# Kernel tuning notes

Hardware: AMD Instinct MI355X
Metric: run time of the kernel (lower is better)

Reference implementation:

```python
import jax, jax.numpy as jnp
import numpy as np

EPS = 1e-5  # nn.BatchNorm2d default eps


def _cbs(x, w, g, b, m, v):
    # Conv(k=1, bias=False) + BatchNorm2d(inference) + SiLU
    y = jnp.einsum('bchw,oc->bohw', x, w)
    s = (g * jax.lax.rsqrt(v + EPS))[None, :, None, None]
    y = (y - m[None, :, None, None]) * s + b[None, :, None, None]
    return y * jax.nn.sigmoid(y)


def setup_inputs():
    key = jax.random.key(0)
    B, D, H, W = 1, 256, 80, 80
    C = D // 2
    ks = jax.random.split(key, 20)
    r = lambda i, shape, sc=1.0: jax.random.normal(ks[i], shape, dtype=jnp.float32) * sc
    oC, oD = jnp.ones((C,), jnp.float32), jnp.ones((D,), jnp.float32)
    zC, zD = jnp.zeros((C,), jnp.float32), jnp.zeros((D,), jnp.float32)
    return {
        'x': r(0, (B, D, H, W)),
        'w1': r(1, (C, D), 0.05), 'g1': oC, 'b1': zC, 'm1': zC, 'v1': oC,
        'w2': r(2, (D, C), 0.05), 'g2': oD, 'b2': zD, 'm2': zD, 'v2': oD,
        'w3': r(3, (D, C), 0.05), 'g3': oD, 'b3': zD, 'm3': zD, 'v3': oD,
        'wq': r(4, (C, C), 0.05), 'bq': r(5, (C,), 0.01),
        'wk': r(6, (C, C), 0.05), 'bk': r(7, (C,), 0.01),
        'wv': r(8, (C, C), 0.05), 'bv': r(9, (C,), 0.01),
        'wp': r(10, (C, C), 0.05), 'bp': r(11, (C,), 0.01),
        'rel_h': r(12, (1, C, H, 1)), 'rel_w': r(13, (1, C, 1, W)),
        'ef_h': r(14, (1, C, H, 1)), 'ef_w': r(15, (1, C, 1, W)),
    }


def reference(x, w1, g1, b1, m1, v1, w2, g2, b2, m2, v2, w3, g3, b3, m3, v3,
              wq, bq, wk, bk, wv, bv, wp, bp, rel_h, rel_w, ef_h, ef_w):
    x1 = _cbs(x, w1, g1, b1, m1, v1)            # [B, C, H, W]
    B, C, H, W = x1.shape
    HW = H * W
    proj = lambda w, b: (jnp.einsum('bchw,oc->bohw', x1, w)
                         + b[None, :, None, None]).reshape(B, C, HW)
    q = proj(wq, bq)
    k = proj(wk, bk)
    v = proj(wv, bv)
    p = proj(wp, bp)
    # content-content + content-position attention branch
    cp = (rel_h + rel_w).reshape(C, HW)          # [C, HW]
    cc = jnp.einsum('bci,bcj->bij', q, k)        # [B, HW, HW]
    cpos = jnp.einsum('ci,bcj->bij', cp, q)      # [B, HW, HW]
    attn = jax.nn.softmax(cc + cpos, axis=-1)
    # out1[b,c,i] = sum_j v[b,c,j] * attn[b,i,j]  (bmm(v, attn^T))
    out1 = jnp.einsum('bcj,bij->bci', v, attn).reshape(B, C, H, W)
    # extra positional branch (valid because B == 1)
    ef = (ef_h + ef_w).reshape(B, C, HW)         # [1, C, HW]
    ce = jnp.einsum('bci,bcj->bij', p, ef)       # [B, HW, HW]
    eng = jax.nn.softmax(ce, axis=-1)
    out2 = jnp.einsum('bcj,bij->bci', ef, eng).reshape(B, C, H, W)
    return x + _cbs(out1, w2, g2, b2, m2, v2) + _cbs(out2, w3, g3, b3, m3, v3)
```

## Files before the change

kernel.cpp:

```cpp
#include <hip/hip_runtime.h>


typedef unsigned short u16;
typedef __attribute__((ext_vector_type(8))) short bf16x8;
typedef __attribute__((ext_vector_type(4))) float f32x4;
typedef __attribute__((ext_vector_type(4))) unsigned int u32x4;

#define HW 6400
#define BN_EPS 1e-5f

__device__ __forceinline__ u16 f2b(float f) {
  unsigned u = __float_as_uint(f);
  u += 0x7fffu + ((u >> 16) & 1u);
  return (u16)(u >> 16);
}
__device__ __forceinline__ unsigned pack2(float a, float b) {
  return (unsigned)f2b(a) | ((unsigned)f2b(b) << 16);
}
__device__ __forceinline__ f32x4 MFMA(bf16x8 a, bf16x8 b, f32x4 c) {
  return __builtin_amdgcn_mfma_f32_16x16x32_bf16(a, b, c, 0, 0, 0);
}
__device__ __forceinline__ float silu_f(float y) {
  return y / (1.0f + __expf(-y));
}
__device__ __forceinline__ bf16x8 pack8(f32x4 lo, f32x4 hi, float sc) {
  union { bf16x8 v; uint4 u; } r;
  r.u.x = pack2(lo[0] * sc, lo[1] * sc);
  r.u.y = pack2(lo[2] * sc, lo[3] * sc);
  r.u.z = pack2(hi[0] * sc, hi[1] * sc);
  r.u.w = pack2(hi[2] * sc, hi[3] * sc);
  return r.v;
}
__device__ __forceinline__ void gload_lds16(const u16* src, u16* dst) {
  __builtin_amdgcn_global_load_lds(
      (const __attribute__((address_space(1))) void*)src,
      (__attribute__((address_space(3))) void*)dst, 16, 0, 0);
}
__device__ __forceinline__ void lds_fence() {
  __builtin_amdgcn_sched_barrier(0);
  asm volatile("s_waitcnt lgkmcnt(0)" ::: "memory");
  __builtin_amdgcn_sched_barrier(0);
}

__global__ void prep_all(
    const float* __restrict__ rel_h, const float* __restrict__ rel_w,
    const float* __restrict__ ef_h, const float* __restrict__ ef_w,
    const float* __restrict__ w1, const float* __restrict__ g1, const float* __restrict__ b1,
    const float* __restrict__ m1, const float* __restrict__ v1,
    const float* __restrict__ w2, const float* __restrict__ g2, const float* __restrict__ b2,
    const float* __restrict__ m2, const float* __restrict__ v2,
    const float* __restrict__ w3, const float* __restrict__ g3, const float* __restrict__ b3,
    const float* __restrict__ m3, const float* __restrict__ v3,
    const float* __restrict__ wq, const float* __restrict__ bq,
    const float* __restrict__ wk, const float* __restrict__ bk,
    const float* __restrict__ wv, const float* __restrict__ bv,
    const float* __restrict__ wp, const float* __restrict__ bp,
    u16* __restrict__ LT,
    u16* __restrict__ w1b, float* __restrict__ b1e,
    u16* __restrict__ Wcat, float* __restrict__ bcat,
    u16* __restrict__ w2b, float* __restrict__ b2e,
    u16* __restrict__ w3b, float* __restrict__ b3e,
    u16* __restrict__ efhT, u16* __restrict__ efwT,
    u16* __restrict__ efhB, u16* __restrict__ efwB,
    u16* __restrict__ expA, u16* __restrict__ expB,
    float* __restrict__ lbuf)
{
  const int b = blockIdx.x;
  const int t = threadIdx.x;
  if (b < 80) {
    const int h = b;
    const int c0 = (t & 63) * 2;
    const float rh0 = rel_h[c0 * 80 + h], rh1 = rel_h[(c0 + 1) * 80 + h];
    for (int wcol = (t >> 6); wcol < 80; wcol += 4) {
      const int i = h * 80 + wcol;
      float rw0 = rel_w[c0 * 80 + wcol], rw1 = rel_w[(c0 + 1) * 80 + wcol];
      *(unsigned*)&LT[(size_t)i * 256 + 128 + c0] = pack2(rh0 + rw0, rh1 + rw1);
    }
  } else if (b < 144) {
    const int tid = (b - 80) * 256 + t;
    const int stride = 64 * 256;
    for (int idx = tid; idx < 128 * 256; idx += stride) {
      int o = idx >> 8;
      float s = g1[o] * rsqrtf(v1[o] + BN_EPS);
      w1b[idx] = f2b(w1[idx] * s);
    }
    for (int idx = tid; idx < 128; idx += stride) {
      float s = g1[idx] * rsqrtf(v1[idx] + BN_EPS);
      b1e[idx] = b1[idx] - m1[idx] * s;
    }
    for (int idx = tid; idx < 4 * 128 * 128; idx += stride) {
      int which = idx >> 14, r = idx & 16383;
      const float* src = which == 0 ? wq : which == 1 ? wk : which == 2 ? wv : wp;
      Wcat[idx] = f2b(src[r]);
    }
    for (int idx = tid; idx < 512; idx += stride) {
      int which = idx >> 7, r = idx & 127;
      const float* src = which == 0 ? bq : which == 1 ? bk : which == 2 ? bv : bp;
      bcat[idx] = src[r];
    }
    for (int idx = tid; idx < 256 * 128; idx += stride) {
      int o = idx >> 7;
      float s2 = g2[o] * rsqrtf(v2[o] + BN_EPS);
      w2b[idx] = f2b(w2[idx] * s2);
      float s3 = g3[o] * rsqrtf(v3[o] + BN_EPS);
      w3b[idx] = f2b(w3[idx] * s3);
    }
    for (int idx = tid; idx < 256; idx += stride) {
      float s2 = g2[idx] * rsqrtf(v2[idx] + BN_EPS);
      b2e[idx] = b2[idx] - m2[idx] * s2;
      float s3 = g3[idx] * rsqrtf(v3[idx] + BN_EPS);
      b3e[idx] = b3[idx] - m3[idx] * s3;
    }
    for (int idx = tid; idx < 80 * 128; idx += stride) {
      int hj = idx >> 7, c = idx & 127;
      efhT[idx] = f2b(ef_h[c * 80 + hj]);
      efwT[idx] = f2b(ef_w[c * 80 + hj]);
    }
    for (int idx = tid; idx < 128 * 96; idx += stride) {
      int c = idx / 96, hj = idx % 96;
      efhB[idx] = hj < 80 ? f2b(ef_h[c * 80 + hj]) : (u16)0;
      efwB[idx] = hj < 80 ? f2b(ef_w[c * 80 + hj]) : (u16)0;
    }
  } else {
    const int tid = (b - 144) * 256 + t;
    const int stride = 32 * 256;
    for (int idx = tid; idx < HW / 4; idx += stride)
      ((f32x4*)lbuf)[idx] = (f32x4){0.f, 0.f, 0.f, 0.f};
    for (int idx = tid; idx < HW * 96 / 8; idx += stride) {
      ((u32x4*)expA)[idx] = (u32x4){0, 0, 0, 0};
      ((u32x4*)expB)[idx] = (u32x4){0, 0, 0, 0};
    }
  }
}

__global__ __launch_bounds__(128) void front_k(
    const float* __restrict__ x,
    const u16* __restrict__ w1b, const float* __restrict__ b1e,
    const u16* __restrict__ Wcat, const float* __restrict__ bcat,
    u16* __restrict__ LT, u16* __restrict__ RT, u16* __restrict__ Vv,
    u16* __restrict__ pT)
{
  __shared__ __align__(16) u16 tr[2][16][136];
  const int t = threadIdx.x, w = t >> 6, lane = t & 63, jl = lane & 15, q = lane >> 4;
  const int i0 = blockIdx.x * 32 + w * 16;

  bf16x8 afr[8];
#pragma unroll
  for (int ks = 0; ks < 8; ++ks) {
    union { bf16x8 v; u16 e[8]; } fa;
#pragma unroll
    for (int e = 0; e < 8; ++e)
      fa.e[e] = f2b(x[(size_t)(ks * 32 + q * 8 + e) * HW + i0 + jl]);
    afr[ks] = fa.v;
  }
  f32x4 acc[8];
#pragma unroll
  for (int nf = 0; nf < 8; ++nf) acc[nf] = (f32x4){0.f, 0.f, 0.f, 0.f};
#pragma unroll
  for (int ks = 0; ks < 8; ++ks)
#pragma unroll
    for (int nf = 0; nf < 8; ++nf) {
      bf16x8 b = *(const bf16x8*)(w1b + (size_t)(nf * 16 + jl) * 256 + ks * 32 + q * 8);
      acc[nf] = MFMA(afr[ks], b, acc[nf]);
    }
#pragma unroll
  for (int nf = 0; nf < 8; ++nf) {
    const int c = nf * 16 + jl;
    const float bias = b1e[c];
#pragma unroll
    for (int r = 0; r < 4; ++r)
      tr[w][q * 4 + r][c] = f2b(silu_f(acc[nf][r] + bias));
  }
  __syncthreads();
  bf16x8 xa[4];
#pragma unroll
  for (int ks = 0; ks < 4; ++ks)
    xa[ks] = *(const bf16x8*)&tr[w][jl][ks * 32 + q * 8];

#pragma unroll
  for (int nc = 0; nc < 4; ++nc) {
    f32x4 a2[8];
#pragma unroll
    for (int nf = 0; nf < 8; ++nf) a2[nf] = (f32x4){0.f, 0.f, 0.f, 0.f};
#pragma unroll
    for (int ks = 0; ks < 4; ++ks)
#pragma unroll
      for (int nf = 0; nf < 8; ++nf) {
        bf16x8 b = *(const bf16x8*)(Wcat + (size_t)(nc * 128 + nf * 16 + jl) * 128 + ks * 32 + q * 8);
        a2[nf] = MFMA(xa[ks], b, a2[nf]);
      }
    if (nc == 2) {
#pragma unroll
      for (int nf = 0; nf < 8; ++nf) {
        const int c = nf * 16 + jl;
        const float bias = bcat[256 + c];
        uint2 pk;
        pk.x = pack2(a2[nf][0] + bias, a2[nf][1] + bias);
        pk.y = pack2(a2[nf][2] + bias, a2[nf][3] + bias);
        *(uint2*)(Vv + (size_t)c * HW + i0 + q * 4) = pk;
      }
    } else {
      __syncthreads();
#pragma unroll
      for (int nf = 0; nf < 8; ++nf) {
        const int c = nf * 16 + jl;
        const float bias = bcat[nc * 128 + c];
#pragma unroll
        for (int r = 0; r < 4; ++r)
          tr[w][q * 4 + r][c] = f2b(a2[nf][r] + bias);
      }
      __syncthreads();
#pragma unroll
      for (int r = 0; r < 16; ++r) {
        unsigned val = *(const unsigned*)&tr[w][r][lane * 2];
        const size_t row = (size_t)(i0 + r);
        if (nc == 0) {
          *(unsigned*)(LT + row * 256 + lane * 2) = val;
          *(unsigned*)(RT + row * 256 + 128 + lane * 2) = val;
        } else if (nc == 1) {
          *(unsigned*)(RT + row * 256 + lane * 2) = val;
        } else {
          *(unsigned*)(pT + row * 128 + lane * 2) = val;
        }
      }
    }
  }
}

__global__ __launch_bounds__(256) void sep2a(
    const u16* __restrict__ pT,
    const u16* __restrict__ efhT,
    const u16* __restrict__ efwT,
    u16* __restrict__ expA, u16* __restrict__ expB,
    float* __restrict__ sA, float* __restrict__ sB)
{
  const int t = threadIdx.x, lane = t & 63, w = t >> 6, jl = lane & 15, q = lane >> 4;
  const int i0w = blockIdx.x * 128 + w * 32;

  bf16x8 pfr[2][4];
#pragma unroll
  for (int mt = 0; mt < 2; ++mt)
#pragma unroll
    for (int l = 0; l < 4; ++l)
      pfr[mt][l] = *(const bf16x8*)(pT + (size_t)(i0w + mt * 16 + jl) * 128 + l * 32 + q * 8);

  f32x4 sa[5][2], sb[5][2];
#pragma unroll
  for (int nf = 0; nf < 5; ++nf)
#pragma unroll
    for (int mt = 0; mt < 2; ++mt) {
      sa[nf][mt] = (f32x4){0.f, 0.f, 0.f, 0.f};
      sb[nf][mt] = (f32x4){0.f, 0.f, 0.f, 0.f};
    }
#pragma unroll
  for (int nf = 0; nf < 5; ++nf) {
    const int row = nf * 16 + jl;
#pragma unroll
    for (int l = 0; l < 4; ++l) {
      bf16x8 eh = *(const bf16x8*)(efhT + (size_t)row * 128 + l * 32 + q * 8);
      bf16x8 ew = *(const bf16x8*)(efwT + (size_t)row * 128 + l * 32 + q * 8);
      sa[nf][0] = MFMA(eh, pfr[0][l], sa[nf][0]);
      sa[nf][1] = MFMA(eh, pfr[1][l], sa[nf][1]);
      sb[nf][0] = MFMA(ew, pfr[0][l], sb[nf][0]);
      sb[nf][1] = MFMA(ew, pfr[1][l], sb[nf][1]);
    }
  }
#pragma unroll
  for (int mt = 0; mt < 2; ++mt) {
    const int i = i0w + mt * 16 + jl;
    float ra = 0.f, rb = 0.f;
#pragma unroll
    for (int nf = 0; nf < 5; ++nf) {
      float ea[4], eb[4];
#pragma unroll
      for (int r = 0; r < 4; ++r) {
        ea[r] = __expf(sa[nf][mt][r]); ra += ea[r];
        eb[r] = __expf(sb[nf][mt][r]); rb += eb[r];
      }
      uint2 pa, pb;
      pa.x = pack2(ea[0], ea[1]); pa.y = pack2(ea[2], ea[3]);
      pb.x = pack2(eb[0], eb[1]); pb.y = pack2(eb[2], eb[3]);
      *(uint2*)(expA + (size_t)i * 96 + nf * 16 + q * 4) = pa;
      *(uint2*)(expB + (size_t)i * 96 + nf * 16 + q * 4) = pb;
    }
    ra += __shfl_xor(ra, 16); ra += __shfl_xor(ra, 32);
    rb += __shfl_xor(rb, 16); rb += __shfl_xor(rb, 32);
    if (lane < 16) { sA[i] = ra; sB[i] = rb; }
  }
}

__global__ __launch_bounds__(256) void sep2b(
    const u16* __restrict__ expA, const u16* __restrict__ expB,
    const float* __restrict__ sA, const float* __restrict__ sB,
    const u16* __restrict__ efhB, const u16* __restrict__ efwB,
    float* __restrict__ O2)
{
  const int t = threadIdx.x, lane = t & 63, w = t >> 6, jl = lane & 15, q = lane >> 4;
  const int i0w = blockIdx.x * 128 + w * 32;

#pragma unroll
  for (int mt = 0; mt < 2; ++mt) {
    bf16x8 fa[3], fb[3];
#pragma unroll
    for (int l = 0; l < 3; ++l) {
      fa[l] = *(const bf16x8*)(expA + (size_t)(i0w + mt * 16 + jl) * 96 + l * 32 + q * 8);
      fb[l] = *(const bf16x8*)(expB + (size_t)(i0w + mt * 16 + jl) * 96 + l * 32 + q * 8);
    }
    f32x4 oU[8], oW[8];
#pragma unroll
    for (int nf = 0; nf < 8; ++nf) {
      oU[nf] = (f32x4){0.f, 0.f, 0.f, 0.f};
      oW[nf] = (f32x4){0.f, 0.f, 0.f, 0.f};
    }
#pragma unroll
    for (int l = 0; l < 3; ++l)
#pragma unroll
      for (int nf = 0; nf < 8; ++nf) {
        bf16x8 bh = *(const bf16x8*)(efhB + (size_t)(nf * 16 + jl) * 96 + l * 32 + q * 8);
        bf16x8 bw = *(const bf16x8*)(efwB + (size_t)(nf * 16 + jl) * 96 + l * 32 + q * 8);
        oU[nf] = MFMA(fa[l], bh, oU[nf]);
        oW[nf] = MFMA(fb[l], bw, oW[nf]);
      }
    const int ib = i0w + mt * 16 + q * 4;
    float ia[4], iw[4];
#pragma unroll
    for (int r = 0; r < 4; ++r) {
      ia[r] = 1.0f / sA[ib + r];
      iw[r] = 1.0f / sB[ib + r];
    }
#pragma unroll
    for (int nf = 0; nf < 8; ++nf)
#pragma unroll
      for (int r = 0; r < 4; ++r)
        O2[(size_t)(ib + r) * 128 + nf * 16 + jl] = oU[nf][r] * ia[r] + oW[nf][r] * iw[r];
  }
}

__global__ __launch_bounds__(512) void fused_attn(
    const u16* __restrict__ LT,
    const u16* __restrict__ RT,
    const u16* __restrict__ Vv,
    float* __restrict__ Opart,
    float* __restrict__ lv)
{
  __shared__ __align__(1024) u16 Rs[2][128 * 128];
  __shared__ __align__(1024) u16 Ts[8][32 * 128];
  const int t = threadIdx.x, lane = t & 63, w = t >> 6, jl = lane & 15, q = lane >> 4;
  const int it = blockIdx.x / 10, jp = blockIdx.x % 10;
  const int i0w = it * 256 + w * 32;
  u16* T0 = Ts[w];
  u16* T1 = Ts[w] + 2048;

  bf16x8 afr[2][8];
#pragma unroll
  for (int mt = 0; mt < 2; ++mt)
#pragma unroll
    for (int l = 0; l < 8; ++l)
      afr[mt][l] = *(const bf16x8*)(LT + (size_t)(i0w + mt * 16 + jl) * 256 + l * 32 + q * 8);

  f32x4 o[2][8];
#pragma unroll
  for (int mt = 0; mt < 2; ++mt)
#pragma unroll
    for (int cf = 0; cf < 8; ++cf) o[mt][cf] = (f32x4){0.f, 0.f, 0.f, 0.f};
  float lacc[2] = {0.f, 0.f};

  auto stage = [&](int jj) {
#pragma unroll
    for (int k = 0; k < 8; ++k) {
      const int b = k >> 2, cl = k & 3;
      const int cc = w * 4 + cl;
      const int jr = cc * 4 + (lane >> 4);
      const int cp = lane & 15;
      const int ch = (cp & ~7) | ((cp ^ jr) & 7);
      gload_lds16(RT + (size_t)(jj + jr) * 256 + b * 128 + ch * 8,
                  Rs[b] + (cc << 9));
    }
  };

  stage(jp * 640);

  for (int stp = 0; stp < 5; ++stp) {
    const int jj = jp * 640 + stp * 128;

    f32x4 s[8][2];
#pragma unroll
    for (int nf = 0; nf < 8; ++nf)
#pragma unroll
      for (int mt = 0; mt < 2; ++mt) s[nf][mt] = (f32x4){0.f, 0.f, 0.f, 0.f};

    __syncthreads();

#pragma unroll
    for (int h = 0; h < 2; ++h)
#pragma unroll
      for (int nf = 0; nf < 8; ++nf) {
        const int row = nf * 16 + jl;
#pragma unroll
        for (int l = 0; l < 4; ++l) {
          const int ch = (l * 4 + q) ^ (jl & 7);
          bf16x8 b = *(const bf16x8*)(Rs[h] + row * 128 + ch * 8);
          s[nf][0] = MFMA(b, afr[0][h * 4 + l], s[nf][0]);
          s[nf][1] = MFMA(b, afr[1][h * 4 + l], s[nf][1]);
        }
      }
    __syncthreads();
    if (stp < 4) stage(jj + 128);

#pragma unroll
    for (int nf = 0; nf < 8; ++nf)
#pragma unroll
      for (int mt = 0; mt < 2; ++mt)
#pragma unroll
        for (int r = 0; r < 4; ++r) {
          float p = __expf(s[nf][mt][r]);
          s[nf][mt][r] = p;
          lacc[mt] += p;
        }

#pragma unroll
    for (int mt = 0; mt < 2; ++mt)
#pragma unroll
      for (int nf = 0; nf < 8; ++nf) {
        const int cs = (nf * 4 + q) ^ ((jl & 7) << 2);
        uint2 pk;
        pk.x = pack2(s[nf][mt][0], s[nf][mt][1]);
        pk.y = pack2(s[nf][mt][2], s[nf][mt][3]);
        *(uint2*)((mt ? T1 : T0) + jl * 128 + cs * 4) = pk;
      }
    lds_fence();

#pragma unroll
    for (int ks2 = 0; ks2 < 4; ++ks2) {
      const int cb = (ks2 * 8 + q * 2) ^ ((jl & 7) << 2);
      bf16x8 pa0 = *(const bf16x8*)(T0 + jl * 128 + cb * 4);
      bf16x8 pa1 = *(const bf16x8*)(T1 + jl * 128 + cb * 4);
#pragma unroll
      for (int cf = 0; cf < 8; ++cf) {
        bf16x8 bv = *(const bf16x8*)(Vv + (size_t)(cf * 16 + jl) * HW + jj + ks2 * 32 + q * 8);
        o[0][cf] = MFMA(pa0, bv, o[0][cf]);
        o[1][cf] = MFMA(pa1, bv, o[1][cf]);
      }
    }
  }

#pragma unroll
  for (int mt = 0; mt < 2; ++mt) {
    float rsum = lacc[mt];
    rsum += __shfl_xor(rsum, 16);
    rsum += __shfl_xor(rsum, 32);
    if (lane < 16)
      atomicAdd(&lv[i0w + mt * 16 + jl], rsum);
  }
  float* Op = Opart + (size_t)jp * HW * 128;
#pragma unroll
  for (int mt = 0; mt < 2; ++mt) {
    const int ib = i0w + mt * 16 + q * 4;
#pragma unroll
    for (int cf = 0; cf < 8; ++cf) {
      const int c = cf * 16 + jl;
#pragma unroll
      for (int r = 0; r < 4; ++r)
        Op[(size_t)(ib + r) * 128 + c] = o[mt][cf][r];
    }
  }
}

__global__ __launch_bounds__(256) void final_k(
    const float* __restrict__ Opart,
    const float* __restrict__ O2,
    const float* __restrict__ lbuf,
    const u16* __restrict__ w2b, const float* __restrict__ b2e,
    const u16* __restrict__ w3b, const float* __restrict__ b3e,
    const float* __restrict__ x, float* __restrict__ outp)
{
  const int t = threadIdx.x, w = t >> 6, lane = t & 63, jl = lane & 15, q = lane >> 4;
  const int i0 = blockIdx.x * 64 + w * 16;
  const int nc = blockIdx.y;
  const int row = i0 + jl;

  const float inv1 = 1.0f / lbuf[row];
  const float* O2r = O2 + (size_t)row * 128;

  f32x4 a1[8], a2[8];
#pragma unroll
  for (int nf = 0; nf < 8; ++nf) {
    a1[nf] = (f32x4){0.f, 0.f, 0.f, 0.f};
    a2[nf] = (f32x4){0.f, 0.f, 0.f, 0.f};
  }
#pragma unroll
  for (int ks = 0; ks < 4; ++ks) {
    f32x4 s1a = (f32x4){0.f, 0.f, 0.f, 0.f};
    f32x4 s1b = (f32x4){0.f, 0.f, 0.f, 0.f};
#pragma unroll
    for (int p = 0; p < 10; ++p) {
      const float* Or = Opart + ((size_t)p * HW + row) * 128;
      s1a += *(const f32x4*)(Or + ks * 32 + q * 8);
      s1b += *(const f32x4*)(Or + ks * 32 + q * 8 + 4);
    }
    f32x4 s2a = *(const f32x4*)(O2r + ks * 32 + q * 8);
    f32x4 s2b = *(const f32x4*)(O2r + ks * 32 + q * 8 + 4);
    bf16x8 fa1 = pack8(s1a, s1b, inv1);
    bf16x8 fa2 = pack8(s2a, s2b, 1.0f);
#pragma unroll
    for (int nf = 0; nf < 8; ++nf) {
      bf16x8 b2f = *(const bf16x8*)(w2b + (size_t)(nc * 128 + nf * 16 + jl) * 128 + ks * 32 + q * 8);
      bf16x8 b3f = *(const bf16x8*)(w3b + (size_t)(nc * 128 + nf * 16 + jl) * 128 + ks * 32 + q * 8);
      a1[nf] = MFMA(fa1, b2f, a1[nf]);
      a2[nf] = MFMA(fa2, b3f, a2[nf]);
    }
  }
#pragma unroll
  for (int nf = 0; nf < 8; ++nf) {
    const int d = nc * 128 + nf * 16 + jl;
    const float bb2 = b2e[d], bb3 = b3e[d];
    const size_t base = (size_t)d * HW + i0 + q * 4;
    f32x4 xv = *(const f32x4*)(x + base);
    f32x4 rv;
#pragma unroll
    for (int r = 0; r < 4; ++r)
      rv[r] = xv[r] + silu_f(a1[nf][r] + bb2) + silu_f(a2[nf][r] + bb3);
    *(f32x4*)(outp + base) = rv;
  }
}

extern "C" void kernel_launch(void* const* d_in, const int* in_sizes, int n_in,
                              void* d_out, int out_size, void* d_ws, size_t ws_size,
                              hipStream_t stream)
{
  (void)in_sizes; (void)n_in; (void)out_size; (void)ws_size;
  const float* x   = (const float*)d_in[0];
  const float* w1  = (const float*)d_in[1];
  const float* g1  = (const float*)d_in[2];
  const float* b1  = (const float*)d_in[3];
  const float* m1  = (const float*)d_in[4];
  const float* v1  = (const float*)d_in[5];
  const float* w2  = (const float*)d_in[6];
  const float* g2  = (const float*)d_in[7];
  const float* b2  = (const float*)d_in[8];
  const float* m2  = (const float*)d_in[9];
  const float* v2  = (const float*)d_in[10];
  const float* w3  = (const float*)d_in[11];
  const float* g3  = (const float*)d_in[12];
  const float* b3  = (const float*)d_in[13];
  const float* m3  = (const float*)d_in[14];
  const float* v3  = (const float*)d_in[15];
  const float* wq  = (const float*)d_in[16];
  const float* bq  = (const float*)d_in[17];
  const float* wk  = (const float*)d_in[18];
  const float* bk  = (const float*)d_in[19];
  const float* wv  = (const float*)d_in[20];
  const float* bv  = (const float*)d_in[21];
  const float* wp  = (const float*)d_in[22];
  const float* bp  = (const float*)d_in[23];
  const float* rel_h = (const float*)d_in[24];
  const float* rel_w = (const float*)d_in[25];
  const float* ef_h  = (const float*)d_in[26];
  const float* ef_w  = (const float*)d_in[27];
  float* outp = (float*)d_out;

  char* ws = (char*)d_ws;
  size_t off = 0;
  auto alloc = [&](size_t bytes) -> void* {
    void* p = ws + off;
    off += (bytes + 511) & ~(size_t)511;
    return p;
  };
  u16* LT    = (u16*)alloc((size_t)HW * 256 * 2);
  u16* RT    = (u16*)alloc((size_t)HW * 256 * 2);
  u16* pT    = (u16*)alloc((size_t)HW * 128 * 2);
  u16* Vv    = (u16*)alloc((size_t)HW * 128 * 2);
  float* Opart = (float*)alloc((size_t)10 * HW * 128 * 4);
  float* O2    = (float*)alloc((size_t)HW * 128 * 4);
  float* lbuf  = (float*)alloc((size_t)HW * 4);
  u16* w1b   = (u16*)alloc(128 * 256 * 2);
  float* b1e = (float*)alloc(128 * 4);
  u16* Wcat  = (u16*)alloc(512 * 128 * 2);
  float* bcat = (float*)alloc(512 * 4);
  u16* w2b   = (u16*)alloc(256 * 128 * 2);
  float* b2e = (float*)alloc(256 * 4);
  u16* w3b   = (u16*)alloc(256 * 128 * 2);
  float* b3e = (float*)alloc(256 * 4);
  u16* efhT  = (u16*)alloc(80 * 128 * 2);
  u16* efwT  = (u16*)alloc(80 * 128 * 2);
  u16* efhB  = (u16*)alloc(128 * 96 * 2);
  u16* efwB  = (u16*)alloc(128 * 96 * 2);
  u16* expA  = (u16*)alloc((size_t)HW * 96 * 2);
  u16* expB  = (u16*)alloc((size_t)HW * 96 * 2);
  float* sA  = (float*)alloc(HW * 4);
  float* sB  = (float*)alloc(HW * 4);

  prep_all<<<176, 256, 0, stream>>>(rel_h, rel_w, ef_h, ef_w,
                                    w1, g1, b1, m1, v1, w2, g2, b2, m2, v2,
                                    w3, g3, b3, m3, v3, wq, bq, wk, bk, wv, bv, wp, bp,
                                    LT, w1b, b1e, Wcat, bcat, w2b, b2e, w3b, b3e,
                                    efhT, efwT, efhB, efwB, expA, expB, lbuf);
  front_k<<<200, 128, 0, stream>>>(x, w1b, b1e, Wcat, bcat, LT, RT, Vv, pT);
  sep2a<<<50, 256, 0, stream>>>(pT, efhT, efwT, expA, expB, sA, sB);
  sep2b<<<50, 256, 0, stream>>>(expA, expB, sA, sB, efhB, efwB, O2);
  fused_attn<<<250, 512, 0, stream>>>(LT, RT, Vv, Opart, lbuf);
  final_k<<<dim3(100, 2), 256, 0, stream>>>(Opart, O2, lbuf, w2b, b2e, w3b, b3e, x, outp);
}
```

Measured before the change: 256.1 us.

## Retile fused attention warps, split front kernel, add separate partial-sum reduction kernel

Reorganizes fused_attn so its 8 waves form a 2x4 grid over 64 query rows and 32-column slices, sharing a per-row-group P tile in LDS with block syncs. Each block now covers 128 query rows, the grid doubles, and the kernel requests 2 blocks per CU. The 10-way partial-output reduction and normalization move out of final_k into a new red_k kernel that writes bf16, and sep2b now writes its output as bf16. front_k is shrunk to one wave per block with twice as many blocks. The aim is better occupancy and register use in attention and less redundant fp32 traffic in final_k, at the cost of an extra kernel launch and an extra pass over Opart.

Result: faster. 249.9 us (-2.4%).

```diff
diff --git a/kernel.cpp b/kernel.cpp
--- a/kernel.cpp
+++ b/kernel.cpp
@@ -35,11 +35,6 @@
   __builtin_amdgcn_global_load_lds(
       (const __attribute__((address_space(1))) void*)src,
       (__attribute__((address_space(3))) void*)dst, 16, 0, 0);
-}
-__device__ __forceinline__ void lds_fence() {
-  __builtin_amdgcn_sched_barrier(0);
-  asm volatile("s_waitcnt lgkmcnt(0)" ::: "memory");
-  __builtin_amdgcn_sched_barrier(0);
 }
 
 __global__ void prep_all(
@@ -133,16 +128,16 @@
   }
 }
 
-__global__ __launch_bounds__(128) void front_k(
+__global__ __launch_bounds__(64) void front_k(
     const float* __restrict__ x,
     const u16* __restrict__ w1b, const float* __restrict__ b1e,
     const u16* __restrict__ Wcat, const float* __restrict__ bcat,
     u16* __restrict__ LT, u16* __restrict__ RT, u16* __restrict__ Vv,
     u16* __restrict__ pT)
 {
-  __shared__ __align__(16) u16 tr[2][16][136];
-  const int t = threadIdx.x, w = t >> 6, lane = t & 63, jl = lane & 15, q = lane >> 4;
-  const int i0 = blockIdx.x * 32 + w * 16;
+  __shared__ __align__(16) u16 tr[16][136];
+  const int t = threadIdx.x, lane = t & 63, jl = lane & 15, q = lane >> 4;
+  const int i0 = blockIdx.x * 16;
 
   bf16x8 afr[8];
 #pragma unroll
@@ -169,13 +164,13 @@
     const float bias = b1e[c];
 #pragma unroll
     for (int r = 0; r < 4; ++r)
-      tr[w][q * 4 + r][c] = f2b(silu_f(acc[nf][r] + bias));
+      tr[q * 4 + r][c] = f2b(silu_f(acc[nf][r] + bias));
   }
   __syncthreads();
   bf16x8 xa[4];
 #pragma unroll
   for (int ks = 0; ks < 4; ++ks)
-    xa[ks] = *(const bf16x8*)&tr[w][jl][ks * 32 + q * 8];
+    xa[ks] = *(const bf16x8*)&tr[jl][ks * 32 + q * 8];
 
 #pragma unroll
   for (int nc = 0; nc < 4; ++nc) {
@@ -207,12 +202,12 @@
         const float bias = bcat[nc * 128 + c];
 #pragma unroll
         for (int r = 0; r < 4; ++r)
-          tr[w][q * 4 + r][c] = f2b(a2[nf][r] + bias);
+          tr[q * 4 + r][c] = f2b(a2[nf][r] + bias);
       }
       __syncthreads();
 #pragma unroll
       for (int r = 0; r < 16; ++r) {
-        unsigned val = *(const unsigned*)&tr[w][r][lane * 2];
+        unsigned val = *(const unsigned*)&tr[r][lane * 2];
         const size_t row = (size_t)(i0 + r);
         if (nc == 0) {
           *(unsigned*)(LT + row * 256 + lane * 2) = val;
@@ -293,7 +288,7 @@
     const u16* __restrict__ expA, const u16* __restrict__ expB,
     const float* __restrict__ sA, const float* __restrict__ sB,
     const u16* __restrict__ efhB, const u16* __restrict__ efwB,
-    float* __restrict__ O2)
+    u16* __restrict__ Ob2)
 {
   const int t = threadIdx.x, lane = t & 63, w = t >> 6, jl = lane & 15, q = lane >> 4;
   const int i0w = blockIdx.x * 128 + w * 32;
@@ -332,11 +327,12 @@
     for (int nf = 0; nf < 8; ++nf)
 #pragma unroll
       for (int r = 0; r < 4; ++r)
-        O2[(size_t)(ib + r) * 128 + nf * 16 + jl] = oU[nf][r] * ia[r] + oW[nf][r] * iw[r];
-  }
-}
-
-__global__ __launch_bounds__(512) void fused_attn(
+        Ob2[(size_t)(ib + r) * 128 + nf * 16 + jl] =
+            f2b(oU[nf][r] * ia[r] + oW[nf][r] * iw[r]);
+  }
+}
+
+__global__ __launch_bounds__(512, 2) void fused_attn(
     const u16* __restrict__ LT,
     const u16* __restrict__ RT,
     const u16* __restrict__ Vv,
@@ -344,26 +340,26 @@
     float* __restrict__ lv)
 {
   __shared__ __align__(1024) u16 Rs[2][128 * 128];
-  __shared__ __align__(1024) u16 Ts[8][32 * 128];
+  __shared__ __align__(1024) u16 Ts[2][64 * 128];
   const int t = threadIdx.x, lane = t & 63, w = t >> 6, jl = lane & 15, q = lane >> 4;
   const int it = blockIdx.x / 10, jp = blockIdx.x % 10;
-  const int i0w = it * 256 + w * 32;
-  u16* T0 = Ts[w];
-  u16* T1 = Ts[w] + 2048;
-
-  bf16x8 afr[2][8];
-#pragma unroll
-  for (int mt = 0; mt < 2; ++mt)
+  const int wi = w & 1, wj = w >> 1;
+  const int i0w = it * 128 + wi * 64;
+  u16* Tw = Ts[wi];
+
+  bf16x8 afr[4][8];
+#pragma unroll
+  for (int mt = 0; mt < 4; ++mt)
 #pragma unroll
     for (int l = 0; l < 8; ++l)
       afr[mt][l] = *(const bf16x8*)(LT + (size_t)(i0w + mt * 16 + jl) * 256 + l * 32 + q * 8);
 
-  f32x4 o[2][8];
-#pragma unroll
-  for (int mt = 0; mt < 2; ++mt)
-#pragma unroll
-    for (int cf = 0; cf < 8; ++cf) o[mt][cf] = (f32x4){0.f, 0.f, 0.f, 0.f};
-  float lacc[2] = {0.f, 0.f};
+  f32x4 o[4][2];
+#pragma unroll
+  for (int mt = 0; mt < 4; ++mt)
+#pragma unroll
+    for (int cf = 0; cf < 2; ++cf) o[mt][cf] = (f32x4){0.f, 0.f, 0.f, 0.f};
+  float lacc[4] = {0.f, 0.f, 0.f, 0.f};
 
   auto stage = [&](int jj) {
 #pragma unroll
@@ -383,34 +379,36 @@
   for (int stp = 0; stp < 5; ++stp) {
     const int jj = jp * 640 + stp * 128;
 
-    f32x4 s[8][2];
-#pragma unroll
-    for (int nf = 0; nf < 8; ++nf)
-#pragma unroll
-      for (int mt = 0; mt < 2; ++mt) s[nf][mt] = (f32x4){0.f, 0.f, 0.f, 0.f};
+    f32x4 s[2][4];
+#pragma unroll
+    for (int nf = 0; nf < 2; ++nf)
+#pragma unroll
+      for (int mt = 0; mt < 4; ++mt) s[nf][mt] = (f32x4){0.f, 0.f, 0.f, 0.f};
 
     __syncthreads();
 
 #pragma unroll
     for (int h = 0; h < 2; ++h)
 #pragma unroll
-      for (int nf = 0; nf < 8; ++nf) {
-        const int row = nf * 16 + jl;
+      for (int nf = 0; nf < 2; ++nf) {
+        const int row = wj * 32 + nf * 16 + jl;
 #pragma unroll
         for (int l = 0; l < 4; ++l) {
           const int ch = (l * 4 + q) ^ (jl & 7);
           bf16x8 b = *(const bf16x8*)(Rs[h] + row * 128 + ch * 8);
           s[nf][0] = MFMA(b, afr[0][h * 4 + l], s[nf][0]);
           s[nf][1] = MFMA(b, afr[1][h * 4 + l], s[nf][1]);
+          s[nf][2] = MFMA(b, afr[2][h * 4 + l], s[nf][2]);
+          s[nf][3] = MFMA(b, afr[3][h * 4 + l], s[nf][3]);
         }
       }
     __syncthreads();
     if (stp < 4) stage(jj + 128);
 
 #pragma unroll
-    for (int nf = 0; nf < 8; ++nf)
-#pragma unroll
-      for (int mt = 0; mt < 2; ++mt)
+    for (int nf = 0; nf < 2; ++nf)
+#pragma unroll
+      for (int mt = 0; mt < 4; ++mt)
 #pragma unroll
         for (int r = 0; r < 4; ++r) {
           float p = __expf(s[nf][mt][r]);
@@ -419,33 +417,34 @@
         }
 
 #pragma unroll
-    for (int mt = 0; mt < 2; ++mt)
-#pragma unroll
-      for (int nf = 0; nf < 8; ++nf) {
-        const int cs = (nf * 4 + q) ^ ((jl & 7) << 2);
+    for (int mt = 0; mt < 4; ++mt)
+#pragma unroll
+      for (int nf = 0; nf < 2; ++nf) {
+        const int row = mt * 16 + jl;
+        const int cs = (wj * 8 + nf * 4 + q) ^ ((jl & 7) << 2);
         uint2 pk;
         pk.x = pack2(s[nf][mt][0], s[nf][mt][1]);
         pk.y = pack2(s[nf][mt][2], s[nf][mt][3]);
-        *(uint2*)((mt ? T1 : T0) + jl * 128 + cs * 4) = pk;
-      }
-    lds_fence();
+        *(uint2*)(Tw + row * 128 + cs * 4) = pk;
+      }
+    __syncthreads();
 
 #pragma unroll
     for (int ks2 = 0; ks2 < 4; ++ks2) {
+      bf16x8 bv0 = *(const bf16x8*)(Vv + (size_t)(wj * 32 + jl) * HW + jj + ks2 * 32 + q * 8);
+      bf16x8 bv1 = *(const bf16x8*)(Vv + (size_t)(wj * 32 + 16 + jl) * HW + jj + ks2 * 32 + q * 8);
       const int cb = (ks2 * 8 + q * 2) ^ ((jl & 7) << 2);
-      bf16x8 pa0 = *(const bf16x8*)(T0 + jl * 128 + cb * 4);
-      bf16x8 pa1 = *(const bf16x8*)(T1 + jl * 128 + cb * 4);
-#pragma unroll
-      for (int cf = 0; cf < 8; ++cf) {
-        bf16x8 bv = *(const bf16x8*)(Vv + (size_t)(cf * 16 + jl) * HW + jj + ks2 * 32 + q * 8);
-        o[0][cf] = MFMA(pa0, bv, o[0][cf]);
-        o[1][cf] = MFMA(pa1, bv, o[1][cf]);
-      }
-    }
-  }
-
-#pragma unroll
-  for (int mt = 0; mt < 2; ++mt) {
+#pragma unroll
+      for (int mt = 0; mt < 4; ++mt) {
+        bf16x8 pa = *(const bf16x8*)(Tw + (mt * 16 + jl) * 128 + cb * 4);
+        o[mt][0] = MFMA(pa, bv0, o[mt][0]);
+        o[mt][1] = MFMA(pa, bv1, o[mt][1]);
+      }
+    }
+  }
+
+#pragma unroll
+  for (int mt = 0; mt < 4; ++mt) {
     float rsum = lacc[mt];
     rsum += __shfl_xor(rsum, 16);
     rsum += __shfl_xor(rsum, 32);
@@ -454,11 +453,11 @@
   }
   float* Op = Opart + (size_t)jp * HW * 128;
 #pragma unroll
-  for (int mt = 0; mt < 2; ++mt) {
+  for (int mt = 0; mt < 4; ++mt) {
     const int ib = i0w + mt * 16 + q * 4;
 #pragma unroll
-    for (int cf = 0; cf < 8; ++cf) {
-      const int c = cf * 16 + jl;
+    for (int cf = 0; cf < 2; ++cf) {
+      const int c = wj * 32 + cf * 16 + jl;
 #pragma unroll
       for (int r = 0; r < 4; ++r)
         Op[(size_t)(ib + r) * 128 + c] = o[mt][cf][r];
@@ -466,10 +465,28 @@
   }
 }
 
+__global__ __launch_bounds__(256) void red_k(
+    const float* __restrict__ Opart,
+    const float* __restrict__ lv,
+    u16* __restrict__ Ob1)
+{
+  const int idx = blockIdx.x * 256 + threadIdx.x;
+  const int i = idx >> 4;
+  const int c0 = (idx & 15) * 8;
+  f32x4 a = {0.f, 0.f, 0.f, 0.f}, b = {0.f, 0.f, 0.f, 0.f};
+#pragma unroll
+  for (int p = 0; p < 10; ++p) {
+    const float* src = Opart + ((size_t)p * HW + i) * 128 + c0;
+    a += *(const f32x4*)src;
+    b += *(const f32x4*)(src + 4);
+  }
+  const float inv = 1.0f / lv[i];
+  *(bf16x8*)(Ob1 + (size_t)i * 128 + c0) = pack8(a, b, inv);
+}
+
 __global__ __launch_bounds__(256) void final_k(
-    const float* __restrict__ Opart,
-    const float* __restrict__ O2,
-    const float* __restrict__ lbuf,
+    const u16* __restrict__ Ob1,
+    const u16* __restrict__ Ob2,
     const u16* __restrict__ w2b, const float* __restrict__ b2e,
     const u16* __restrict__ w3b, const float* __restrict__ b3e,
     const float* __restrict__ x, float* __restrict__ outp)
@@ -479,9 +496,6 @@
   const int nc = blockIdx.y;
   const int row = i0 + jl;
 
-  const float inv1 = 1.0f / lbuf[row];
-  const float* O2r = O2 + (size_t)row * 128;
-
   f32x4 a1[8], a2[8];
 #pragma unroll
   for (int nf = 0; nf < 8; ++nf) {
@@ -490,18 +504,8 @@
   }
 #pragma unroll
   for (int ks = 0; ks < 4; ++ks) {
-    f32x4 s1a = (f32x4){0.f, 0.f, 0.f, 0.f};
-    f32x4 s1b = (f32x4){0.f, 0.f, 0.f, 0.f};
-#pragma unroll
-    for (int p = 0; p < 10; ++p) {
-      const float* Or = Opart + ((size_t)p * HW + row) * 128;
-      s1a += *(const f32x4*)(Or + ks * 32 + q * 8);
-      s1b += *(const f32x4*)(Or + ks * 32 + q * 8 + 4);
-    }
-    f32x4 s2a = *(const f32x4*)(O2r + ks * 32 + q * 8);
-    f32x4 s2b = *(const f32x4*)(O2r + ks * 32 + q * 8 + 4);
-    bf16x8 fa1 = pack8(s1a, s1b, inv1);
-    bf16x8 fa2 = pack8(s2a, s2b, 1.0f);
+    bf16x8 fa1 = *(const bf16x8*)(Ob1 + (size_t)row * 128 + ks * 32 + q * 8);
+    bf16x8 fa2 = *(const bf16x8*)(Ob2 + (size_t)row * 128 + ks * 32 + q * 8);
 #pragma unroll
     for (int nf = 0; nf < 8; ++nf) {
       bf16x8 b2f = *(const bf16x8*)(w2b + (size_t)(nc * 128 + nf * 16 + jl) * 128 + ks * 32 + q * 8);
@@ -571,7 +575,8 @@
   u16* pT    = (u16*)alloc((size_t)HW * 128 * 2);
   u16* Vv    = (u16*)alloc((size_t)HW * 128 * 2);
   float* Opart = (float*)alloc((size_t)10 * HW * 128 * 4);
-  float* O2    = (float*)alloc((size_t)HW * 128 * 4);
+  u16* Ob1   = (u16*)alloc((size_t)HW * 128 * 2);
+  u16* Ob2   = (u16*)alloc((size_t)HW * 128 * 2);
   float* lbuf  = (float*)alloc((size_t)HW * 4);
   u16* w1b   = (u16*)alloc(128 * 256 * 2);
   float* b1e = (float*)alloc(128 * 4);
@@ -595,9 +600,10 @@
                                     w3, g3, b3, m3, v3, wq, bq, wk, bk, wv, bv, wp, bp,
                                     LT, w1b, b1e, Wcat, bcat, w2b, b2e, w3b, b3e,
                                     efhT, efwT, efhB, efwB, expA, expB, lbuf);
-  front_k<<<200, 128, 0, stream>>>(x, w1b, b1e, Wcat, bcat, LT, RT, Vv, pT);
+  front_k<<<400, 64, 0, stream>>>(x, w1b, b1e, Wcat, bcat, LT, RT, Vv, pT);
   sep2a<<<50, 256, 0, stream>>>(pT, efhT, efwT, expA, expB, sA, sB);
-  sep2b<<<50, 256, 0, stream>>>(expA, expB, sA, sB, efhB, efwB, O2);
-  fused_attn<<<250, 512, 0, stream>>>(LT, RT, Vv, Opart, lbuf);
-  final_k<<<dim3(100, 2), 256, 0, stream>>>(Opart, O2, lbuf, w2b, b2e, w3b, b3e, x, outp);
-}
+  sep2b<<<50, 256, 0, stream>>>(expA, expB, sA, sB, efhB, efwB, Ob2);
+  fused_attn<<<500, 512, 0, stream>>>(LT, RT, Vv, Opart, lbuf);
+  red_k<<<400, 256, 0, stream>>>(Opart, lbuf, Ob1);
+  final_k<<<dim3(100, 2), 256, 0, stream>>>(Ob1, Ob2, w2b, b2e, w3b, b3e, x, outp);
+}
```

## Retile attention, fold sep2a into attention grid and sep2b into final

Applied to the files above, without the earlier changes.

The attention kernel now uses 64-row query tiles per 256-thread block, with four waves split 2x2 across rows and output channels. A single shared P tile replaces the per-wave transpose buffers, and setprio hints are added around the MFMA sections. The sep2a work runs as extra blocks appended to the attention grid, and the sep2b contraction is fused into the final kernel through LDS, which removes the O2 fp32 round trip and two launches. front_k also moves to 64-thread blocks with twice as many of them. The cost is full-block barriers in place of per-wave fences, and smaller tiles that increase how often RT and Vv are reloaded.

New measurement: 251.6 us. Within noise of the previous version (-1.8%).

```diff
diff --git a/kernel.cpp b/kernel.cpp
--- a/kernel.cpp
+++ b/kernel.cpp
@@ -35,11 +35,6 @@
   __builtin_amdgcn_global_load_lds(
       (const __attribute__((address_space(1))) void*)src,
       (__attribute__((address_space(3))) void*)dst, 16, 0, 0);
-}
-__device__ __forceinline__ void lds_fence() {
-  __builtin_amdgcn_sched_barrier(0);
-  asm volatile("s_waitcnt lgkmcnt(0)" ::: "memory");
-  __builtin_amdgcn_sched_barrier(0);
 }
 
 __global__ void prep_all(
@@ -133,16 +128,16 @@
   }
 }
 
-__global__ __launch_bounds__(128) void front_k(
+__global__ __launch_bounds__(64) void front_k(
     const float* __restrict__ x,
     const u16* __restrict__ w1b, const float* __restrict__ b1e,
     const u16* __restrict__ Wcat, const float* __restrict__ bcat,
     u16* __restrict__ LT, u16* __restrict__ RT, u16* __restrict__ Vv,
     u16* __restrict__ pT)
 {
-  __shared__ __align__(16) u16 tr[2][16][136];
-  const int t = threadIdx.x, w = t >> 6, lane = t & 63, jl = lane & 15, q = lane >> 4;
-  const int i0 = blockIdx.x * 32 + w * 16;
+  __shared__ __align__(16) u16 tr[16][136];
+  const int t = threadIdx.x, lane = t & 63, jl = lane & 15, q = lane >> 4;
+  const int i0 = blockIdx.x * 16;
 
   bf16x8 afr[8];
 #pragma unroll
@@ -169,13 +164,13 @@
     const float bias = b1e[c];
 #pragma unroll
     for (int r = 0; r < 4; ++r)
-      tr[w][q * 4 + r][c] = f2b(silu_f(acc[nf][r] + bias));
+      tr[q * 4 + r][c] = f2b(silu_f(acc[nf][r] + bias));
   }
   __syncthreads();
   bf16x8 xa[4];
 #pragma unroll
   for (int ks = 0; ks < 4; ++ks)
-    xa[ks] = *(const bf16x8*)&tr[w][jl][ks * 32 + q * 8];
+    xa[ks] = *(const bf16x8*)&tr[jl][ks * 32 + q * 8];
 
 #pragma unroll
   for (int nc = 0; nc < 4; ++nc) {
@@ -207,12 +202,12 @@
         const float bias = bcat[nc * 128 + c];
 #pragma unroll
         for (int r = 0; r < 4; ++r)
-          tr[w][q * 4 + r][c] = f2b(a2[nf][r] + bias);
+          tr[q * 4 + r][c] = f2b(a2[nf][r] + bias);
       }
       __syncthreads();
 #pragma unroll
       for (int r = 0; r < 16; ++r) {
-        unsigned val = *(const unsigned*)&tr[w][r][lane * 2];
+        unsigned val = *(const unsigned*)&tr[r][lane * 2];
         const size_t row = (size_t)(i0 + r);
         if (nc == 0) {
           *(unsigned*)(LT + row * 256 + lane * 2) = val;
@@ -227,15 +222,15 @@
   }
 }
 
-__global__ __launch_bounds__(256) void sep2a(
-    const u16* __restrict__ pT,
-    const u16* __restrict__ efhT,
+__device__ __forceinline__ void sep2a_body(
+    int b2,
+    const u16* __restrict__ pT, const u16* __restrict__ efhT,
     const u16* __restrict__ efwT,
     u16* __restrict__ expA, u16* __restrict__ expB,
     float* __restrict__ sA, float* __restrict__ sB)
 {
   const int t = threadIdx.x, lane = t & 63, w = t >> 6, jl = lane & 15, q = lane >> 4;
-  const int i0w = blockIdx.x * 128 + w * 32;
+  const int i0w = b2 * 128 + w * 32;
 
   bf16x8 pfr[2][4];
 #pragma unroll
@@ -289,67 +284,29 @@
   }
 }
 
-__global__ __launch_bounds__(256) void sep2b(
-    const u16* __restrict__ expA, const u16* __restrict__ expB,
-    const float* __restrict__ sA, const float* __restrict__ sB,
-    const u16* __restrict__ efhB, const u16* __restrict__ efwB,
-    float* __restrict__ O2)
-{
-  const int t = threadIdx.x, lane = t & 63, w = t >> 6, jl = lane & 15, q = lane >> 4;
-  const int i0w = blockIdx.x * 128 + w * 32;
-
-#pragma unroll
-  for (int mt = 0; mt < 2; ++mt) {
-    bf16x8 fa[3], fb[3];
-#pragma unroll
-    for (int l = 0; l < 3; ++l) {
-      fa[l] = *(const bf16x8*)(expA + (size_t)(i0w + mt * 16 + jl) * 96 + l * 32 + q * 8);
-      fb[l] = *(const bf16x8*)(expB + (size_t)(i0w + mt * 16 + jl) * 96 + l * 32 + q * 8);
-    }
-    f32x4 oU[8], oW[8];
-#pragma unroll
-    for (int nf = 0; nf < 8; ++nf) {
-      oU[nf] = (f32x4){0.f, 0.f, 0.f, 0.f};
-      oW[nf] = (f32x4){0.f, 0.f, 0.f, 0.f};
-    }
-#pragma unroll
-    for (int l = 0; l < 3; ++l)
-#pragma unroll
-      for (int nf = 0; nf < 8; ++nf) {
-        bf16x8 bh = *(const bf16x8*)(efhB + (size_t)(nf * 16 + jl) * 96 + l * 32 + q * 8);
-        bf16x8 bw = *(const bf16x8*)(efwB + (size_t)(nf * 16 + jl) * 96 + l * 32 + q * 8);
-        oU[nf] = MFMA(fa[l], bh, oU[nf]);
-        oW[nf] = MFMA(fb[l], bw, oW[nf]);
-      }
-    const int ib = i0w + mt * 16 + q * 4;
-    float ia[4], iw[4];
-#pragma unroll
-    for (int r = 0; r < 4; ++r) {
-      ia[r] = 1.0f / sA[ib + r];
-      iw[r] = 1.0f / sB[ib + r];
-    }
-#pragma unroll
-    for (int nf = 0; nf < 8; ++nf)
-#pragma unroll
-      for (int r = 0; r < 4; ++r)
-        O2[(size_t)(ib + r) * 128 + nf * 16 + jl] = oU[nf][r] * ia[r] + oW[nf][r] * iw[r];
-  }
-}
-
-__global__ __launch_bounds__(512) void fused_attn(
+__global__ __launch_bounds__(256, 2) void fused_attn(
     const u16* __restrict__ LT,
     const u16* __restrict__ RT,
     const u16* __restrict__ Vv,
     float* __restrict__ Opart,
-    float* __restrict__ lv)
+    float* __restrict__ lv,
+    const u16* __restrict__ pT, const u16* __restrict__ efhT,
+    const u16* __restrict__ efwT,
+    u16* __restrict__ expA, u16* __restrict__ expB,
+    float* __restrict__ sA, float* __restrict__ sB)
 {
   __shared__ __align__(1024) u16 Rs[2][128 * 128];
-  __shared__ __align__(1024) u16 Ts[8][32 * 128];
+  __shared__ __align__(1024) u16 Tb[64 * 128];
+  const int bid = blockIdx.x;
+  if (bid >= 1000) {
+    sep2a_body(bid - 1000, pT, efhT, efwT, expA, expB, sA, sB);
+    return;
+  }
   const int t = threadIdx.x, lane = t & 63, w = t >> 6, jl = lane & 15, q = lane >> 4;
-  const int it = blockIdx.x / 10, jp = blockIdx.x % 10;
-  const int i0w = it * 256 + w * 32;
-  u16* T0 = Ts[w];
-  u16* T1 = Ts[w] + 2048;
+  const int it = bid / 10, jp = bid % 10;
+  const int wi = w & 1, wj = w >> 1;
+  const int i0b = it * 64;
+  const int i0w = i0b + wi * 32;
 
   bf16x8 afr[2][8];
 #pragma unroll
@@ -358,23 +315,23 @@
     for (int l = 0; l < 8; ++l)
       afr[mt][l] = *(const bf16x8*)(LT + (size_t)(i0w + mt * 16 + jl) * 256 + l * 32 + q * 8);
 
-  f32x4 o[2][8];
+  f32x4 o[2][4];
 #pragma unroll
   for (int mt = 0; mt < 2; ++mt)
 #pragma unroll
-    for (int cf = 0; cf < 8; ++cf) o[mt][cf] = (f32x4){0.f, 0.f, 0.f, 0.f};
+    for (int cf = 0; cf < 4; ++cf) o[mt][cf] = (f32x4){0.f, 0.f, 0.f, 0.f};
   float lacc[2] = {0.f, 0.f};
 
   auto stage = [&](int jj) {
 #pragma unroll
-    for (int k = 0; k < 8; ++k) {
-      const int b = k >> 2, cl = k & 3;
-      const int cc = w * 4 + cl;
+    for (int k = 0; k < 16; ++k) {
+      const int bh = k >> 3, cl = k & 7;
+      const int cc = w * 8 + cl;
       const int jr = cc * 4 + (lane >> 4);
       const int cp = lane & 15;
       const int ch = (cp & ~7) | ((cp ^ jr) & 7);
-      gload_lds16(RT + (size_t)(jj + jr) * 256 + b * 128 + ch * 8,
-                  Rs[b] + (cc << 9));
+      gload_lds16(RT + (size_t)(jj + jr) * 256 + bh * 128 + ch * 8,
+                  Rs[bh] + (cc << 9));
     }
   };
 
@@ -383,19 +340,20 @@
   for (int stp = 0; stp < 5; ++stp) {
     const int jj = jp * 640 + stp * 128;
 
-    f32x4 s[8][2];
-#pragma unroll
-    for (int nf = 0; nf < 8; ++nf)
+    f32x4 s[4][2];
+#pragma unroll
+    for (int nf = 0; nf < 4; ++nf)
 #pragma unroll
       for (int mt = 0; mt < 2; ++mt) s[nf][mt] = (f32x4){0.f, 0.f, 0.f, 0.f};
 
     __syncthreads();
 
+    __builtin_amdgcn_s_setprio(1);
 #pragma unroll
     for (int h = 0; h < 2; ++h)
 #pragma unroll
-      for (int nf = 0; nf < 8; ++nf) {
-        const int row = nf * 16 + jl;
+      for (int nf = 0; nf < 4; ++nf) {
+        const int row = wj * 64 + nf * 16 + jl;
 #pragma unroll
         for (int l = 0; l < 4; ++l) {
           const int ch = (l * 4 + q) ^ (jl & 7);
@@ -404,11 +362,12 @@
           s[nf][1] = MFMA(b, afr[1][h * 4 + l], s[nf][1]);
         }
       }
+    __builtin_amdgcn_s_setprio(0);
     __syncthreads();
     if (stp < 4) stage(jj + 128);
 
 #pragma unroll
-    for (int nf = 0; nf < 8; ++nf)
+    for (int nf = 0; nf < 4; ++nf)
 #pragma unroll
       for (int mt = 0; mt < 2; ++mt)
 #pragma unroll
@@ -421,27 +380,30 @@
 #pragma unroll
     for (int mt = 0; mt < 2; ++mt)
 #pragma unroll
-      for (int nf = 0; nf < 8; ++nf) {
-        const int cs = (nf * 4 + q) ^ ((jl & 7) << 2);
+      for (int nf = 0; nf < 4; ++nf) {
+        const int row = wi * 32 + mt * 16 + jl;
+        const int cs = (wj * 16 + nf * 4 + q) ^ ((jl & 7) << 2);
         uint2 pk;
         pk.x = pack2(s[nf][mt][0], s[nf][mt][1]);
         pk.y = pack2(s[nf][mt][2], s[nf][mt][3]);
-        *(uint2*)((mt ? T1 : T0) + jl * 128 + cs * 4) = pk;
-      }
-    lds_fence();
-
+        *(uint2*)(Tb + row * 128 + cs * 4) = pk;
+      }
+    __syncthreads();
+
+    __builtin_amdgcn_s_setprio(1);
 #pragma unroll
     for (int ks2 = 0; ks2 < 4; ++ks2) {
       const int cb = (ks2 * 8 + q * 2) ^ ((jl & 7) << 2);
-      bf16x8 pa0 = *(const bf16x8*)(T0 + jl * 128 + cb * 4);
-      bf16x8 pa1 = *(const bf16x8*)(T1 + jl * 128 + cb * 4);
-#pragma unroll
-      for (int cf = 0; cf < 8; ++cf) {
-        bf16x8 bv = *(const bf16x8*)(Vv + (size_t)(cf * 16 + jl) * HW + jj + ks2 * 32 + q * 8);
+      bf16x8 pa0 = *(const bf16x8*)(Tb + (wi * 32 + jl) * 128 + cb * 4);
+      bf16x8 pa1 = *(const bf16x8*)(Tb + (wi * 32 + 16 + jl) * 128 + cb * 4);
+#pragma unroll
+      for (int cf = 0; cf < 4; ++cf) {
+        bf16x8 bv = *(const bf16x8*)(Vv + (size_t)(wj * 64 + cf * 16 + jl) * HW + jj + ks2 * 32 + q * 8);
         o[0][cf] = MFMA(pa0, bv, o[0][cf]);
         o[1][cf] = MFMA(pa1, bv, o[1][cf]);
       }
     }
+    __builtin_amdgcn_s_setprio(0);
   }
 
 #pragma unroll
@@ -457,8 +419,8 @@
   for (int mt = 0; mt < 2; ++mt) {
     const int ib = i0w + mt * 16 + q * 4;
 #pragma unroll
-    for (int cf = 0; cf < 8; ++cf) {
-      const int c = cf * 16 + jl;
+    for (int cf = 0; cf < 4; ++cf) {
+      const int c = wj * 64 + cf * 16 + jl;
 #pragma unroll
       for (int r = 0; r < 4; ++r)
         Op[(size_t)(ib + r) * 128 + c] = o[mt][cf][r];
@@ -466,22 +428,61 @@
   }
 }
 
-__global__ __launch_bounds__(256) void final_k(
+__global__ __launch_bounds__(256) void final2(
+    const u16* __restrict__ expA, const u16* __restrict__ expB,
+    const float* __restrict__ sA, const float* __restrict__ sB,
+    const u16* __restrict__ efhB, const u16* __restrict__ efwB,
     const float* __restrict__ Opart,
-    const float* __restrict__ O2,
-    const float* __restrict__ lbuf,
+    const float* __restrict__ lv,
     const u16* __restrict__ w2b, const float* __restrict__ b2e,
     const u16* __restrict__ w3b, const float* __restrict__ b3e,
     const float* __restrict__ x, float* __restrict__ outp)
 {
-  const int t = threadIdx.x, w = t >> 6, lane = t & 63, jl = lane & 15, q = lane >> 4;
-  const int i0 = blockIdx.x * 64 + w * 16;
+  __shared__ __align__(16) u16 T2[64][136];
+  const int t = threadIdx.x, lane = t & 63, w = t >> 6, jl = lane & 15, q = lane >> 4;
+  const int i0 = blockIdx.x * 64;
   const int nc = blockIdx.y;
-  const int row = i0 + jl;
-
-  const float inv1 = 1.0f / lbuf[row];
-  const float* O2r = O2 + (size_t)row * 128;
-
+  const int rowA = i0 + w * 16 + jl;
+
+  {
+    bf16x8 fa[3], fb[3];
+#pragma unroll
+    for (int l = 0; l < 3; ++l) {
+      fa[l] = *(const bf16x8*)(expA + (size_t)rowA * 96 + l * 32 + q * 8);
+      fb[l] = *(const bf16x8*)(expB + (size_t)rowA * 96 + l * 32 + q * 8);
+    }
+    f32x4 oU[8], oW[8];
+#pragma unroll
+    for (int nf = 0; nf < 8; ++nf) {
+      oU[nf] = (f32x4){0.f, 0.f, 0.f, 0.f};
+      oW[nf] = (f32x4){0.f, 0.f, 0.f, 0.f};
+    }
+#pragma unroll
+    for (int l = 0; l < 3; ++l)
+#pragma unroll
+      for (int nf = 0; nf < 8; ++nf) {
+        bf16x8 bh = *(const bf16x8*)(efhB + (size_t)(nf * 16 + jl) * 96 + l * 32 + q * 8);
+        bf16x8 bw = *(const bf16x8*)(efwB + (size_t)(nf * 16 + jl) * 96 + l * 32 + q * 8);
+        oU[nf] = MFMA(fa[l], bh, oU[nf]);
+        oW[nf] = MFMA(fb[l], bw, oW[nf]);
+      }
+    const int ib = i0 + w * 16 + q * 4;
+    float ia[4], iw[4];
+#pragma unroll
+    for (int r = 0; r < 4; ++r) {
+      ia[r] = 1.0f / sA[ib + r];
+      iw[r] = 1.0f / sB[ib + r];
+    }
+#pragma unroll
+    for (int nf = 0; nf < 8; ++nf)
+#pragma unroll
+      for (int r = 0; r < 4; ++r)
+        T2[w * 16 + q * 4 + r][nf * 16 + jl] =
+            f2b(oU[nf][r] * ia[r] + oW[nf][r] * iw[r]);
+  }
+  __syncthreads();
+
+  const float inv1 = 1.0f / lv[rowA];
   f32x4 a1[8], a2[8];
 #pragma unroll
   for (int nf = 0; nf < 8; ++nf) {
@@ -494,14 +495,12 @@
     f32x4 s1b = (f32x4){0.f, 0.f, 0.f, 0.f};
 #pragma unroll
     for (int p = 0; p < 10; ++p) {
-      const float* Or = Opart + ((size_t)p * HW + row) * 128;
+      const float* Or = Opart + ((size_t)p * HW + rowA) * 128;
       s1a += *(const f32x4*)(Or + ks * 32 + q * 8);
       s1b += *(const f32x4*)(Or + ks * 32 + q * 8 + 4);
     }
-    f32x4 s2a = *(const f32x4*)(O2r + ks * 32 + q * 8);
-    f32x4 s2b = *(const f32x4*)(O2r + ks * 32 + q * 8 + 4);
     bf16x8 fa1 = pack8(s1a, s1b, inv1);
-    bf16x8 fa2 = pack8(s2a, s2b, 1.0f);
+    bf16x8 fa2 = *(const bf16x8*)&T2[w * 16 + jl][ks * 32 + q * 8];
 #pragma unroll
     for (int nf = 0; nf < 8; ++nf) {
       bf16x8 b2f = *(const bf16x8*)(w2b + (size_t)(nc * 128 + nf * 16 + jl) * 128 + ks * 32 + q * 8);
@@ -514,7 +513,7 @@
   for (int nf = 0; nf < 8; ++nf) {
     const int d = nc * 128 + nf * 16 + jl;
     const float bb2 = b2e[d], bb3 = b3e[d];
-    const size_t base = (size_t)d * HW + i0 + q * 4;
+    const size_t base = (size_t)d * HW + i0 + w * 16 + q * 4;
     f32x4 xv = *(const f32x4*)(x + base);
     f32x4 rv;
 #pragma unroll
@@ -571,7 +570,6 @@
   u16* pT    = (u16*)alloc((size_t)HW * 128 * 2);
   u16* Vv    = (u16*)alloc((size_t)HW * 128 * 2);
   float* Opart = (float*)alloc((size_t)10 * HW * 128 * 4);
-  float* O2    = (float*)alloc((size_t)HW * 128 * 4);
   float* lbuf  = (float*)alloc((size_t)HW * 4);
   u16* w1b   = (u16*)alloc(128 * 256 * 2);
   float* b1e = (float*)alloc(128 * 4);
@@ -595,9 +593,10 @@
                                     w3, g3, b3, m3, v3, wq, bq, wk, bk, wv, bv, wp, bp,
                                     LT, w1b, b1e, Wcat, bcat, w2b, b2e, w3b, b3e,
                                     efhT, efwT, efhB, efwB, expA, expB, lbuf);
-  front_k<<<200, 128, 0, stream>>>(x, w1b, b1e, Wcat, bcat, LT, RT, Vv, pT);
-  sep2a<<<50, 256, 0, stream>>>(pT, efhT, efwT, expA, expB, sA, sB);
-  sep2b<<<50, 256, 0, stream>>>(expA, expB, sA, sB, efhB, efwB, O2);
-  fused_attn<<<250, 512, 0, stream>>>(LT, RT, Vv, Opart, lbuf);
-  final_k<<<dim3(100, 2), 256, 0, stream>>>(Opart, O2, lbuf, w2b, b2e, w3b, b3e, x, outp);
-}
+  front_k<<<400, 64, 0, stream>>>(x, w1b, b1e, Wcat, bcat, LT, RT, Vv, pT);
+  fused_attn<<<1050, 256, 0, stream>>>(LT, RT, Vv, Opart, lbuf,
+                                       pT, efhT, efwT, expA, expB, sA, sB);
+  final2<<<dim3(100, 2), 256, 0, stream>>>(expA, expB, sA, sB, efhB, efwB,
+                                           Opart, lbuf, w2b, b2e, w3b, b3e,
+                                           x, outp);
+}
```
